# Kernel optimization log

Measured on AMD Instinct MI355X. Metric: run time of the kernel, lower is better.

## Reference

```python
import jax, jax.numpy as jnp
import numpy as np

GRID_SIZE = 5
SPLINE_ORDER = 3
GRID_RANGE = (-1.0, 1.0)


def _make_grid():
    # knots: arange(-k, G+k+1)*h + lo, shared across in_features (uniform grid)
    h = (GRID_RANGE[1] - GRID_RANGE[0]) / GRID_SIZE
    return (jnp.arange(-SPLINE_ORDER, GRID_SIZE + SPLINE_ORDER + 1, dtype=jnp.float32) * h
            + GRID_RANGE[0])  # (G + 2k + 1,) = (12,)


def _b_splines(x2d, grid):
    # x2d: (T, C); grid: (12,) broadcast over features
    x = x2d[..., None]  # (T, C, 1)
    g = grid[None, None, :]  # (1, 1, 12)
    bases = ((x >= g[..., :-1]) & (x < g[..., 1:])).astype(x2d.dtype)
    for k in range(1, SPLINE_ORDER + 1):
        left = (x - g[..., : -(k + 1)]) / (g[..., k:-1] - g[..., : -(k + 1)])
        right = (g[..., k + 1:] - x) / (g[..., k + 1:] - g[..., 1:-k])
        bases = left * bases[..., :-1] + right * bases[..., 1:]
    return bases  # (T, C, G + k) = (T, C, 8)


def setup_inputs() -> dict:
    key = jax.random.key(0)
    k1, k2, k3, k4 = jax.random.split(key, 4)
    B, N, C, O = 4, 4096, 768, 768
    n_coef = GRID_SIZE + SPLINE_ORDER  # 8
    x = jax.random.normal(k1, (B, N, C), dtype=jnp.float32) * 0.5
    base_weight = jax.random.normal(k2, (O, C), dtype=jnp.float32) * (1.0 / np.sqrt(C))
    spline_weight = jax.random.normal(k3, (O, C, n_coef), dtype=jnp.float32) * 0.1
    spline_scaler = jax.random.normal(k4, (O, C), dtype=jnp.float32) * (1.0 / np.sqrt(C))
    return {"x": x, "base_weight": base_weight, "spline_weight": spline_weight,
            "spline_scaler": spline_scaler}


def reference(x, base_weight, spline_weight, spline_scaler):
    B, N, C = x.shape
    x2d = x.reshape(B * N, C)
    grid = _make_grid()
    # base path: SiLU activation + linear
    base_out = jnp.einsum('tc,oc->to', jax.nn.silu(x2d), base_weight)
    # spline path: B-spline bases + scaled linear combination
    bases = _b_splines(x2d, grid)  # (T, C, 8)
    w = spline_weight * spline_scaler[..., None]  # (O, C, 8)
    spline_out = jnp.einsum('tcg,ocg->to', bases, w)
    out = (base_out + spline_out).reshape(B, N, -1)
    return out  # dropout with p=0.0 is identity
```

## Files before the change

kernel.cpp:

```cpp
#include <hip/hip_runtime.h>

typedef __attribute__((ext_vector_type(8)))  short  short8;
typedef __attribute__((ext_vector_type(16))) float  f32x16;
typedef __attribute__((ext_vector_type(4)))  float  flt4;
typedef __attribute__((ext_vector_type(2)))  float  flt2;
typedef __attribute__((ext_vector_type(4)))  unsigned int u32x4;

#define T_DIM 16384
#define C_DIM 768
#define O_DIM 768

#define CK2    16
#define CHUNKS 48
#define KSTEPS 9
#define NSG    432
#define K3     6912
#define LDA3   152
#define BM     64
#define BN     768
#define LDSBUF 19456
#define WT3_BYTES  ((size_t)NSG * 12288 * 2)

__device__ __forceinline__ unsigned short f2bf(float f) {
  unsigned u = __float_as_uint(f);
  return (unsigned short)((u + 0x7FFFu + ((u >> 16) & 1u)) >> 16);
}

__device__ __forceinline__ unsigned cvtpk(float lo, float hi) {
  unsigned r;
  asm("v_cvt_pk_bf16_f32 %0, %1, %2" : "=v"(r) : "v"(lo), "v"(hi));
  return r;
}

__global__ void kan_prep3(const float* __restrict__ bw, const float* __restrict__ sw,
                          const float* __restrict__ sc, unsigned short* __restrict__ wt) {
  int id = blockIdx.x * 256 + threadIdx.x;
  if (id >= O_DIM * C_DIM) return;
  int o = id / C_DIM;
  int c = id - o * C_DIM;
  float b = bw[id];
  float s = sc[id];
  const float* sp = sw + (size_t)id * 8;
  {
    int k = (c >> 4) * 144 + (c & 15);
    wt[(size_t)(k >> 4) * 12288 + o * 16 + (k & 15)] = f2bf(b);
  }
#pragma unroll
  for (int g = 0; g < 8; ++g) {
    int k = (c >> 4) * 144 + 16 + (c & 15) * 8 + g;
    wt[(size_t)(k >> 4) * 12288 + o * 16 + (k & 15)] = f2bf(sp[g] * s);
  }
}

__global__ __launch_bounds__(768, 3) void kan_gemm9(
    const float* __restrict__ x, const unsigned short* __restrict__ wt,
    float* __restrict__ out) {
  __shared__ short Alds[2 * BM * LDA3];

  const int tid  = threadIdx.x;
  const int lane = tid & 63;
  const int wn   = tid >> 6;
  const int l31  = lane & 31;
  const int lq   = lane >> 5;

  const int d  = blockIdx.x;
  const int tBase = d * BM;
  const int oBase = wn * 64;

  f32x16 acc[2][2];
#pragma unroll
  for (int a = 0; a < 2; ++a)
#pragma unroll
    for (int b = 0; b < 2; ++b)
#pragma unroll
      for (int r = 0; r < 16; ++r) acc[a][b][r] = 0.0f;

  const bool doStage = (tid < 512);
  const int sRow = (tid >> 3) & 63;
  const int sSb  = tid & 7;
  const float* xrow = x + (size_t)(tBase + sRow) * C_DIM + sSb * 2;

  char* ldsB = (char*)Alds;
  const int wbase = sRow * 304;
  int rbyte[2];
#pragma unroll
  for (int mf = 0; mf < 2; ++mf)
    rbyte[mf] = (mf * 32 + l31) * 304 + lq * 16;

  flt2 xa = *(const flt2*)(xrow);
  float    su[2];
  unsigned sww[8];

  auto stage_j = [&](int j) {
    float xx  = xa[j];
    float ex  = __expf(-xx);
    float sig = __builtin_amdgcn_rcpf(1.0f + ex);
    su[j] = xx * sig;
    float u  = fmaf(xx, 2.5f, 5.5f);
    float fl = floorf(u);
    int   jj = (int)fl;
    float f  = u - fl;
    float f2 = f * f, f3 = f2 * f;
    float W0 = f3 * (1.0f / 6.0f);
    float om = 1.0f - f;
    float W3 = om * om * om * (1.0f / 6.0f);
    float W2 = 0.5f * f3 - f2 + (2.0f / 3.0f);
    float W1 = 1.0f - W0 - W2 - W3;
    unsigned V0 = cvtpk(W3, W2);
    unsigned V1 = cvtpk(W1, W0);
    unsigned A0 = V0 << 16;
    unsigned A1 = (V1 << 16) | (V0 >> 16);
    unsigned A2 = V1 >> 16;
    int  k = jj - 3;
    int  q = k >> 1;
    bool r = (k & 1) != 0;
    unsigned U0 = r ? A0 : V0;
    unsigned U1 = r ? A1 : V1;
    unsigned U2 = r ? A2 : 0u;
#pragma unroll
    for (int p = 0; p < 4; ++p)
      sww[4 * j + p] =
          (q == p) ? U0 : ((q == p - 1) ? U1 : ((q == p - 2) ? U2 : 0u));
  };

#define WRITE_ONE(WR, WOFF)                                             \
  {                                                                     \
    if ((WR) == 0) {                                                    \
      *(unsigned*)(ldsB + (WOFF) + wbase + sSb * 4) = cvtpk(su[0], su[1]); \
    } else {                                                            \
      u32x4 t;                                                          \
      t.x = sww[4 * ((WR) - 1)];     t.y = sww[4 * ((WR) - 1) + 1];     \
      t.z = sww[4 * ((WR) - 1) + 2]; t.w = sww[4 * ((WR) - 1) + 3];     \
      *(u32x4*)(ldsB + (WOFF) + wbase + 32 + sSb * 32 + ((WR) - 1) * 16) = t; \
    }                                                                   \
  }

  if (doStage) {
    stage_j(0); stage_j(1);
    WRITE_ONE(0, 0) WRITE_ONE(1, 0) WRITE_ONE(2, 0)
    xa = *(const flt2*)(xrow + CK2);
  }

  const size_t lofs = (size_t)(oBase + l31) * 16 + lq * 8;
  short8 bb0[2], bb1[2], bb2[2];
  {
    const unsigned short* w0 = wt + lofs;
    bb0[0] = *(const short8*)(w0);
    bb0[1] = *(const short8*)(w0 + 512);
    const unsigned short* w1 = wt + 12288 + lofs;
    bb1[0] = *(const short8*)(w1);
    bb1[1] = *(const short8*)(w1 + 512);
    const unsigned short* w2 = wt + 24576 + lofs;
    bb2[0] = *(const short8*)(w2);
    bb2[1] = *(const short8*)(w2 + 512);
  }
  __syncthreads();

#define LDSA(MF, KS) (*(const short8*)(ldsB + roff + rbyte[MF] + (KS) * 32))
#define MFMA(A, B, C) __builtin_amdgcn_mfma_f32_32x32x16_bf16((A), (B), (C), 0, 0, 0)

  short8 aa0[2], aa1[2];

#define KSTEP(KS, BB, AAC, AAN, DOREAD, SJ, WR, DOX, GUARD)              \
  {                                                                      \
    if (DOREAD) {                                                        \
      AAN[0] = LDSA(0, (KS) + 1);                                        \
      AAN[1] = LDSA(1, (KS) + 1);                                        \
    }                                                                    \
    __builtin_amdgcn_s_setprio(1);                                       \
    acc[0][0] = MFMA(AAC[0], BB[0], acc[0][0]);                          \
    acc[0][1] = MFMA(AAC[0], BB[1], acc[0][1]);                          \
    acc[1][0] = MFMA(AAC[1], BB[0], acc[1][0]);                          \
    acc[1][1] = MFMA(AAC[1], BB[1], acc[1][1]);                          \
    __builtin_amdgcn_s_setprio(0);                                       \
    if (!(GUARD) || (chBase + (KS) + 3 < NSG)) {                         \
      const unsigned short* wp =                                         \
          wt + (size_t)(chBase + (KS) + 3) * 12288 + lofs;               \
      BB[0] = *(const short8*)(wp);                                      \
      BB[1] = *(const short8*)(wp + 512);                                \
    }                                                                    \
    if ((WR) >= 0 && doStage) WRITE_ONE(WR, woff)                        \
    if ((SJ) >= 0 && doStage) stage_j(SJ);                               \
    if ((DOX) && doStage) xa = *(const flt2*)(xrow + (ch + 2) * CK2);    \
  }

  for (int ch = 0; ch < CHUNKS - 1; ++ch) {
    const int chBase = ch * KSTEPS;
    const int roff   = (ch & 1) * LDSBUF;
    const int woff   = roff ^ LDSBUF;
    const bool dox   = (ch + 2 < CHUNKS);
    aa0[0] = LDSA(0, 0);
    aa0[1] = LDSA(1, 0);
    KSTEP(0, bb0, aa0, aa1, 1,  0, -1, false, 0)
    KSTEP(1, bb1, aa1, aa0, 1,  1, -1, false, 0)
    KSTEP(2, bb2, aa0, aa1, 1, -1, -1, dox,   0)
    KSTEP(3, bb0, aa1, aa0, 1, -1, -1, false, 0)
    KSTEP(4, bb1, aa0, aa1, 1, -1,  0, false, 0)
    KSTEP(5, bb2, aa1, aa0, 1, -1,  1, false, 0)
    KSTEP(6, bb0, aa0, aa1, 1, -1,  2, false, 0)
    KSTEP(7, bb1, aa1, aa0, 1, -1, -1, false, 0)
    KSTEP(8, bb2, aa0, aa1, 0, -1, -1, false, 0)
    __syncthreads();
  }
  {
    const int ch     = CHUNKS - 1;
    (void)ch;
    const int chBase = (CHUNKS - 1) * KSTEPS;
    const int roff   = ((CHUNKS - 1) & 1) * LDSBUF;
    const int woff   = 0;
    (void)woff;
    aa0[0] = LDSA(0, 0);
    aa0[1] = LDSA(1, 0);
    KSTEP(0, bb0, aa0, aa1, 1, -1, -1, false, 1)
    KSTEP(1, bb1, aa1, aa0, 1, -1, -1, false, 1)
    KSTEP(2, bb2, aa0, aa1, 1, -1, -1, false, 1)
    KSTEP(3, bb0, aa1, aa0, 1, -1, -1, false, 1)
    KSTEP(4, bb1, aa0, aa1, 1, -1, -1, false, 1)
    KSTEP(5, bb2, aa1, aa0, 1, -1, -1, false, 1)
    KSTEP(6, bb0, aa0, aa1, 1, -1, -1, false, 1)
    KSTEP(7, bb1, aa1, aa0, 1, -1, -1, false, 1)
    KSTEP(8, bb2, aa0, aa1, 0, -1, -1, false, 1)
  }

#undef KSTEP
#undef LDSA
#undef MFMA
#undef WRITE_ONE

#pragma unroll
  for (int mf = 0; mf < 2; ++mf) {
    int tRow0 = tBase + mf * 32 + 4 * lq;
#pragma unroll
    for (int nf = 0; nf < 2; ++nf) {
      int oCol = oBase + nf * 32 + l31;
#pragma unroll
      for (int r = 0; r < 16; ++r) {
        int rowf = (r & 3) + 8 * (r >> 2);
        out[(size_t)(tRow0 + rowf) * O_DIM + oCol] = acc[mf][nf][r];
      }
    }
  }
}

__global__ __launch_bounds__(256, 2) void kan_gemm_fb(
    const float* __restrict__ x, const float* __restrict__ bw,
    const float* __restrict__ sw, const float* __restrict__ sc,
    float* __restrict__ out) {
  __shared__ short Alds[128 * 152];
  const int tid  = threadIdx.x;
  const int lane = tid & 63;
  const int wave = tid >> 6;
  const int wm   = wave >> 1;
  const int wn   = wave & 1;
  const int l31  = lane & 31;
  const int lq   = lane >> 5;
  const int tBase = blockIdx.x * 128;
  const int oBase = blockIdx.y * 192 + wn * 96;
  f32x16 acc[2][3];
#pragma unroll
  for (int a = 0; a < 2; ++a)
#pragma unroll
    for (int b = 0; b < 3; ++b)
#pragma unroll
      for (int r = 0; r < 16; ++r) acc[a][b][r] = 0.0f;
  const int sRow = tid >> 1;
  const int sSb  = tid & 1;
  const float* xrow = x + (size_t)(tBase + sRow) * C_DIM + sSb * 8;
  for (int ch = 0; ch < 48; ++ch) {
    __syncthreads();
    const float* xp = xrow + ch * 16;
    flt4 xv0 = *(const flt4*)(xp);
    flt4 xv1 = *(const flt4*)(xp + 4);
    short8 plane[9];
#pragma unroll
    for (int j = 0; j < 8; ++j) {
      float xx  = (j < 4) ? xv0[j] : xv1[j - 4];
      float sig = 1.0f / (1.0f + __expf(-xx));
      plane[0][j] = f2bf(xx * sig);
      float u  = fmaf(xx, 2.5f, 5.5f);
      float fl = floorf(u);
      int   jj = (int)fl;
      float f  = u - fl;
      float f2 = f * f, f3 = f2 * f;
      float W0 = f3 * (1.0f / 6.0f);
      float om = 1.0f - f;
      float W3 = om * om * om * (1.0f / 6.0f);
      float W2 = 0.5f * f3 - f2 + (2.0f / 3.0f);
      float W1 = 1.0f - W0 - W2 - W3;
#pragma unroll
      for (int s = 0; s < 8; ++s) {
        int   dd  = jj - s;
        float v01 = (dd & 1) ? W1 : W0;
        float v23 = (dd & 1) ? W3 : W2;
        float v   = (dd & 2) ? v23 : v01;
        v = ((unsigned)dd < 4u) ? v : 0.0f;
        plane[1 + s][j] = f2bf(v);
      }
    }
    {
      short* arow = &Alds[sRow * 152 + sSb * 72];
#pragma unroll
      for (int g = 0; g < 9; ++g) *(short8*)(arow + g * 8) = plane[g];
    }
    __syncthreads();
    for (int ks = 0; ks < 9; ++ks) {
      const int sGlob = ch * 9 + ks;
      short8 bfr[3];
      const int h    = sGlob * 2 + lq;
      const int cblk = (h * 7282) >> 16;
      const int g    = h - cblk * 9;
      const int cb   = cblk * 8;
#pragma unroll
      for (int nf = 0; nf < 3; ++nf) {
        int col = oBase + nf * 32 + l31;
        const float* rowb = ((g == 0) ? bw : sc) + (size_t)col * C_DIM + cb;
        flt4 s0 = *(const flt4*)rowb;
        flt4 s1 = *(const flt4*)(rowb + 4);
        short8 v;
        if (g == 0) {
#pragma unroll
          for (int j = 0; j < 8; ++j) v[j] = f2bf((j < 4) ? s0[j] : s1[j - 4]);
        } else {
          const float* sp = sw + ((size_t)col * C_DIM + cb) * 8 + (g - 1);
#pragma unroll
          for (int j = 0; j < 8; ++j) {
            float scv = (j < 4) ? s0[j] : s1[j - 4];
            v[j] = f2bf(sp[j * 8] * scv);
          }
        }
        bfr[nf] = v;
      }
      short8 afr[2];
#pragma unroll
      for (int mf = 0; mf < 2; ++mf)
        afr[mf] = *(const short8*)&Alds[(wm * 64 + mf * 32 + l31) * 152 + ks * 16 + lq * 8];
#pragma unroll
      for (int mf = 0; mf < 2; ++mf)
#pragma unroll
        for (int nf = 0; nf < 3; ++nf)
          acc[mf][nf] = __builtin_amdgcn_mfma_f32_32x32x16_bf16(
              afr[mf], bfr[nf], acc[mf][nf], 0, 0, 0);
    }
  }
#pragma unroll
  for (int mf = 0; mf < 2; ++mf) {
    int tRow0 = tBase + wm * 64 + mf * 32 + 4 * lq;
#pragma unroll
    for (int nf = 0; nf < 3; ++nf) {
      int oCol = oBase + nf * 32 + l31;
#pragma unroll
      for (int r = 0; r < 16; ++r) {
        int rowf = (r & 3) + 8 * (r >> 2);
        out[(size_t)(tRow0 + rowf) * O_DIM + oCol] = acc[mf][nf][r];
      }
    }
  }
}

extern "C" void kernel_launch(void* const* d_in, const int* in_sizes, int n_in,
                              void* d_out, int out_size, void* d_ws, size_t ws_size,
                              hipStream_t stream) {
  const float* x  = (const float*)d_in[0];
  const float* bw = (const float*)d_in[1];
  const float* sw = (const float*)d_in[2];
  const float* sc = (const float*)d_in[3];
  float* out = (float*)d_out;

  const bool use_ws = (d_ws != nullptr) && (ws_size >= WT3_BYTES);
  if (use_ws) {
    unsigned short* wt = (unsigned short*)d_ws;
    kan_prep3<<<(O_DIM * C_DIM + 255) / 256, 256, 0, stream>>>(bw, sw, sc, wt);
    kan_gemm9<<<dim3(T_DIM / BM), 768, 0, stream>>>(x, wt, out);
  } else {
    kan_gemm_fb<<<dim3(T_DIM / 128, O_DIM / 192), 256, 0, stream>>>(x, bw, sw, sc, out);
  }
}
```

Baseline: 169.3 us.

## Shrink GEMM row tile to 32 with 8 waves covering 96 columns each

Reworks the fused KAN GEMM tile from 64 rows × 768 columns with 12 waves (2×2 MFMA tiles each) to 32 rows × 768 columns with 8 waves, each owning a 1×3 tile of 32x32 MFMAs. Weight prefetch depth drops from three register stages to two, and the chunk loop is unrolled by two so LDS buffer offsets become compile-time constants. This doubles the grid and halves LDS per block, aiming for higher occupancy. The cost is each block reloading the full weight matrix for half as many rows, which doubles global and L2 weight traffic.

```diff
diff --git a/kernel.cpp b/kernel.cpp
--- a/kernel.cpp
+++ b/kernel.cpp
@@ -14,11 +14,10 @@
 #define CHUNKS 48
 #define KSTEPS 9
 #define NSG    432
-#define K3     6912
 #define LDA3   152
-#define BM     64
+#define BM     32
 #define BN     768
-#define LDSBUF 19456
+#define LDSBUF 9728
 #define WT3_BYTES  ((size_t)NSG * 12288 * 2)
 
 __device__ __forceinline__ unsigned short f2bf(float f) {
@@ -52,7 +51,7 @@
   }
 }
 
-__global__ __launch_bounds__(768, 3) void kan_gemm9(
+__global__ __launch_bounds__(512, 4) void kan_gemm14(
     const float* __restrict__ x, const unsigned short* __restrict__ wt,
     float* __restrict__ out) {
   __shared__ short Alds[2 * BM * LDA3];
@@ -65,29 +64,24 @@
 
   const int d  = blockIdx.x;
   const int tBase = d * BM;
-  const int oBase = wn * 64;
-
-  f32x16 acc[2][2];
-#pragma unroll
-  for (int a = 0; a < 2; ++a)
-#pragma unroll
-    for (int b = 0; b < 2; ++b)
-#pragma unroll
-      for (int r = 0; r < 16; ++r) acc[a][b][r] = 0.0f;
-
-  const bool doStage = (tid < 512);
-  const int sRow = (tid >> 3) & 63;
+  const int oBase = wn * 96;
+
+  f32x16 acc[3];
+#pragma unroll
+  for (int b = 0; b < 3; ++b)
+#pragma unroll
+    for (int r = 0; r < 16; ++r) acc[b][r] = 0.0f;
+
+  const bool doStage = (tid < 256);
+  const int sRow = (tid >> 3) & 31;
   const int sSb  = tid & 7;
   const float* xrow = x + (size_t)(tBase + sRow) * C_DIM + sSb * 2;
 
   char* ldsB = (char*)Alds;
   const int wbase = sRow * 304;
-  int rbyte[2];
-#pragma unroll
-  for (int mf = 0; mf < 2; ++mf)
-    rbyte[mf] = (mf * 32 + l31) * 304 + lq * 16;
-
-  flt2 xa = *(const flt2*)(xrow);
+  const int rbyte = l31 * 304 + lq * 16;
+
+  flt2 xa;
   float    su[2];
   unsigned sww[8];
 
@@ -136,107 +130,110 @@
   }
 
   if (doStage) {
+    xa = *(const flt2*)(xrow);
     stage_j(0); stage_j(1);
     WRITE_ONE(0, 0) WRITE_ONE(1, 0) WRITE_ONE(2, 0)
     xa = *(const flt2*)(xrow + CK2);
   }
 
   const size_t lofs = (size_t)(oBase + l31) * 16 + lq * 8;
-  short8 bb0[2], bb1[2], bb2[2];
+  short8 bb0[3], bb1[3];
   {
     const unsigned short* w0 = wt + lofs;
     bb0[0] = *(const short8*)(w0);
     bb0[1] = *(const short8*)(w0 + 512);
+    bb0[2] = *(const short8*)(w0 + 1024);
     const unsigned short* w1 = wt + 12288 + lofs;
     bb1[0] = *(const short8*)(w1);
     bb1[1] = *(const short8*)(w1 + 512);
-    const unsigned short* w2 = wt + 24576 + lofs;
-    bb2[0] = *(const short8*)(w2);
-    bb2[1] = *(const short8*)(w2 + 512);
+    bb1[2] = *(const short8*)(w1 + 1024);
   }
   __syncthreads();
 
-#define LDSA(MF, KS) (*(const short8*)(ldsB + roff + rbyte[MF] + (KS) * 32))
+#define LDSA(KS) (*(const short8*)(ldsB + roff + rbyte + (KS) * 32))
 #define MFMA(A, B, C) __builtin_amdgcn_mfma_f32_32x32x16_bf16((A), (B), (C), 0, 0, 0)
 
-  short8 aa0[2], aa1[2];
-
-#define KSTEP(KS, BB, AAC, AAN, DOREAD, SJ, WR, DOX, GUARD)              \
+  short8 aa0, aa1;
+
+#define KSTEP(KS, BB, AAC, AAN, DOREAD, SJ, WR, DOXF, GUARD)             \
   {                                                                      \
-    if (DOREAD) {                                                        \
-      AAN[0] = LDSA(0, (KS) + 1);                                        \
-      AAN[1] = LDSA(1, (KS) + 1);                                        \
-    }                                                                    \
+    if (DOREAD) AAN = LDSA((KS) + 1);                                    \
     __builtin_amdgcn_s_setprio(1);                                       \
-    acc[0][0] = MFMA(AAC[0], BB[0], acc[0][0]);                          \
-    acc[0][1] = MFMA(AAC[0], BB[1], acc[0][1]);                          \
-    acc[1][0] = MFMA(AAC[1], BB[0], acc[1][0]);                          \
-    acc[1][1] = MFMA(AAC[1], BB[1], acc[1][1]);                          \
+    acc[0] = MFMA(AAC, BB[0], acc[0]);                                   \
+    acc[1] = MFMA(AAC, BB[1], acc[1]);                                   \
+    acc[2] = MFMA(AAC, BB[2], acc[2]);                                   \
     __builtin_amdgcn_s_setprio(0);                                       \
-    if (!(GUARD) || (chBase + (KS) + 3 < NSG)) {                         \
+    if (!(GUARD) || (chBase + (KS) + 2 < NSG)) {                         \
       const unsigned short* wp =                                         \
-          wt + (size_t)(chBase + (KS) + 3) * 12288 + lofs;               \
+          wt + (size_t)(chBase + (KS) + 2) * 12288 + lofs;               \
       BB[0] = *(const short8*)(wp);                                      \
       BB[1] = *(const short8*)(wp + 512);                                \
+      BB[2] = *(const short8*)(wp + 1024);                               \
     }                                                                    \
     if ((WR) >= 0 && doStage) WRITE_ONE(WR, woff)                        \
     if ((SJ) >= 0 && doStage) stage_j(SJ);                               \
-    if ((DOX) && doStage) xa = *(const flt2*)(xrow + (ch + 2) * CK2);    \
-  }
-
-  for (int ch = 0; ch < CHUNKS - 1; ++ch) {
-    const int chBase = ch * KSTEPS;
-    const int roff   = (ch & 1) * LDSBUF;
-    const int woff   = roff ^ LDSBUF;
-    const bool dox   = (ch + 2 < CHUNKS);
-    aa0[0] = LDSA(0, 0);
-    aa0[1] = LDSA(1, 0);
-    KSTEP(0, bb0, aa0, aa1, 1,  0, -1, false, 0)
-    KSTEP(1, bb1, aa1, aa0, 1,  1, -1, false, 0)
-    KSTEP(2, bb2, aa0, aa1, 1, -1, -1, dox,   0)
-    KSTEP(3, bb0, aa1, aa0, 1, -1, -1, false, 0)
-    KSTEP(4, bb1, aa0, aa1, 1, -1,  0, false, 0)
-    KSTEP(5, bb2, aa1, aa0, 1, -1,  1, false, 0)
-    KSTEP(6, bb0, aa0, aa1, 1, -1,  2, false, 0)
-    KSTEP(7, bb1, aa1, aa0, 1, -1, -1, false, 0)
-    KSTEP(8, bb2, aa0, aa1, 0, -1, -1, false, 0)
+    if ((DOXF) && doStage) xa = *(const flt2*)(xrow + (ch + 2) * CK2);   \
+  }
+
+#define CHUNK_BODY(B0, B1, STG, DOXF, G)                                 \
+  {                                                                      \
+    aa0 = LDSA(0);                                                       \
+    KSTEP(0, B0, aa0, aa1, 1, (STG) ? 0 : -1, -1, false, G)              \
+    KSTEP(1, B1, aa1, aa0, 1, (STG) ? 1 : -1, -1, false, G)              \
+    KSTEP(2, B0, aa0, aa1, 1, -1, -1, (DOXF), G)                         \
+    KSTEP(3, B1, aa1, aa0, 1, -1, (STG) ? 0 : -1, false, G)              \
+    KSTEP(4, B0, aa0, aa1, 1, -1, (STG) ? 1 : -1, false, G)              \
+    KSTEP(5, B1, aa1, aa0, 1, -1, (STG) ? 2 : -1, false, G)              \
+    KSTEP(6, B0, aa0, aa1, 1, -1, -1, false, G)                          \
+    KSTEP(7, B1, aa1, aa0, 1, -1, -1, false, G)                         \
+    KSTEP(8, B0, aa0, aa1, 0, -1, -1, false, G)                          \
+  }
+
+  for (int p = 0; p < 23; ++p) {
+    {
+      const int ch = 2 * p;
+      const int chBase = ch * KSTEPS;
+      const int roff = 0, woff = LDSBUF;
+      CHUNK_BODY(bb0, bb1, 1, (ch + 2 < CHUNKS), 0)
+      __syncthreads();
+    }
+    {
+      const int ch = 2 * p + 1;
+      const int chBase = ch * KSTEPS;
+      const int roff = LDSBUF, woff = 0;
+      CHUNK_BODY(bb1, bb0, 1, (ch + 2 < CHUNKS), 0)
+      __syncthreads();
+    }
+  }
+  {
+    const int ch = 46;
+    const int chBase = 46 * KSTEPS;
+    const int roff = 0, woff = LDSBUF;
+    CHUNK_BODY(bb0, bb1, 1, false, 0)
     __syncthreads();
   }
   {
-    const int ch     = CHUNKS - 1;
-    (void)ch;
-    const int chBase = (CHUNKS - 1) * KSTEPS;
-    const int roff   = ((CHUNKS - 1) & 1) * LDSBUF;
-    const int woff   = 0;
-    (void)woff;
-    aa0[0] = LDSA(0, 0);
-    aa0[1] = LDSA(1, 0);
-    KSTEP(0, bb0, aa0, aa1, 1, -1, -1, false, 1)
-    KSTEP(1, bb1, aa1, aa0, 1, -1, -1, false, 1)
-    KSTEP(2, bb2, aa0, aa1, 1, -1, -1, false, 1)
-    KSTEP(3, bb0, aa1, aa0, 1, -1, -1, false, 1)
-    KSTEP(4, bb1, aa0, aa1, 1, -1, -1, false, 1)
-    KSTEP(5, bb2, aa1, aa0, 1, -1, -1, false, 1)
-    KSTEP(6, bb0, aa0, aa1, 1, -1, -1, false, 1)
-    KSTEP(7, bb1, aa1, aa0, 1, -1, -1, false, 1)
-    KSTEP(8, bb2, aa0, aa1, 0, -1, -1, false, 1)
-  }
-
+    const int ch = 47; (void)ch;
+    const int chBase = 47 * KSTEPS;
+    const int roff = LDSBUF, woff = 0; (void)woff;
+    CHUNK_BODY(bb1, bb0, 0, false, 1)
+  }
+
+#undef CHUNK_BODY
 #undef KSTEP
 #undef LDSA
 #undef MFMA
 #undef WRITE_ONE
 
-#pragma unroll
-  for (int mf = 0; mf < 2; ++mf) {
-    int tRow0 = tBase + mf * 32 + 4 * lq;
-#pragma unroll
-    for (int nf = 0; nf < 2; ++nf) {
+  {
+    int tRow0 = tBase + 4 * lq;
+#pragma unroll
+    for (int nf = 0; nf < 3; ++nf) {
       int oCol = oBase + nf * 32 + l31;
 #pragma unroll
       for (int r = 0; r < 16; ++r) {
         int rowf = (r & 3) + 8 * (r >> 2);
-        out[(size_t)(tRow0 + rowf) * O_DIM + oCol] = acc[mf][nf][r];
+        out[(size_t)(tRow0 + rowf) * O_DIM + oCol] = acc[nf][r];
       }
     }
   }
@@ -370,7 +367,7 @@
   if (use_ws) {
     unsigned short* wt = (unsigned short*)d_ws;
     kan_prep3<<<(O_DIM * C_DIM + 255) / 256, 256, 0, stream>>>(bw, sw, sc, wt);
-    kan_gemm9<<<dim3(T_DIM / BM), 768, 0, stream>>>(x, wt, out);
+    kan_gemm14<<<dim3(T_DIM / BM), 512, 0, stream>>>(x, wt, out);
   } else {
     kan_gemm_fb<<<dim3(T_DIM / 128, O_DIM / 192), 256, 0, stream>>>(x, bw, sw, sc, out);
   }
```

Result: slower. 219.6 us (+29.7%).
